# Optimization experiments

Hardware: AMD Instinct MI355X
Metric: run time of the kernel (lower is better)

The kernel has to match this reference:

```python
import math
import jax, jax.numpy as jnp
import numpy as np

GROUPS = 32
EPS = 1e-5


def setup_inputs() -> dict:
    key = jax.random.key(0)
    ks = jax.random.split(key, 4)
    B, C, H, W = 32, 512, 32, 32
    x = jax.random.normal(ks[0], (B, C, H, W), dtype=jnp.float32)
    norm_gamma = jnp.ones((C,), dtype=jnp.float32)
    norm_beta = jnp.zeros((C,), dtype=jnp.float32)
    qkv_w = jax.random.normal(ks[1], (3 * C, C), dtype=jnp.float32) / math.sqrt(C)
    qkv_b = jnp.zeros((3 * C,), dtype=jnp.float32)
    proj_w = jax.random.normal(ks[2], (C, C), dtype=jnp.float32) / math.sqrt(C)
    proj_b = jnp.zeros((C,), dtype=jnp.float32)
    return {"x": x, "norm_gamma": norm_gamma, "norm_beta": norm_beta,
            "qkv_w": qkv_w, "qkv_b": qkv_b, "proj_w": proj_w, "proj_b": proj_b}


def _group_norm(x, gamma, beta):
    B, C, H, W = x.shape
    xg = x.reshape(B, GROUPS, C // GROUPS, H, W)
    mean = xg.mean(axis=(2, 3, 4), keepdims=True)
    var = xg.var(axis=(2, 3, 4), keepdims=True)
    xn = ((xg - mean) * jax.lax.rsqrt(var + EPS)).reshape(B, C, H, W)
    return xn * gamma[None, :, None, None] + beta[None, :, None, None]


def reference(x, norm_gamma, norm_beta, qkv_w, qkv_b, proj_w, proj_b):
    B, C, H, W = x.shape
    h = _group_norm(x, norm_gamma, norm_beta)
    # 1x1 conv == channel matmul: [3C, C] x [B, C, H, W] -> [B, 3C, H, W]
    qkv = jnp.einsum('oc,bchw->bohw', qkv_w, h) + qkv_b[None, :, None, None]
    qkv = qkv.reshape(B, 3, C, H * W)
    q, k, v = qkv[:, 0], qkv[:, 1], qkv[:, 2]  # each [B, C, N]
    scale = 1.0 / math.sqrt(math.sqrt(C))
    w = jnp.einsum('bci,bcj->bij', q * scale, k * scale)  # [B, N, N]
    w = jax.nn.softmax(w, axis=-1)
    h = jnp.einsum('bij,bcj->bci', w, v).reshape(B, C, H, W)
    out = x + jnp.einsum('oc,bchw->bohw', proj_w, h) + proj_b[None, :, None, None]
    return out
```

## Files before the change

kernel.cpp:

```cpp
#include <hip/hip_runtime.h>

#define GROUPS 32
#define CPG    16
#define C_DIM  512
#define HW     1024
#define B_DIM  32

typedef __attribute__((ext_vector_type(8))) short bf16x8;
typedef __attribute__((ext_vector_type(4))) float f32x4;
typedef __attribute__((ext_vector_type(8))) unsigned short u16x8;

__device__ inline unsigned short f2bf(float f) {
  unsigned u = __builtin_bit_cast(unsigned, f);
  u += 0x7fff + ((u >> 16) & 1);
  return (unsigned short)(u >> 16);
}
__device__ inline float bf2f(unsigned short s) {
  return __builtin_bit_cast(float, ((unsigned)s) << 16);
}

__device__ inline void mfma16(f32x4& d, bf16x8 a, bf16x8 b) {
  asm("v_mfma_f32_16x16x32_bf16 %0, %1, %2, %0" : "+v"(d) : "v"(a), "v"(b));
}

__device__ inline void stage128x64(const unsigned short* g0, size_t rowStride,
                                   unsigned short* lds, int wave, int lane) {
  int r  = lane >> 3;
  int k8 = (lane & 7) * 8;
#pragma unroll
  for (int i = 0; i < 4; ++i) {
    const unsigned short* g = g0 + (size_t)(wave * 32 + i * 8 + r) * rowStride + k8;
    unsigned short* l = lds + (wave * 32 + i * 8) * 64;
    __builtin_amdgcn_global_load_lds((const __attribute__((address_space(1))) void*)g,
                                     (__attribute__((address_space(3))) void*)l, 16, 0, 0);
  }
}

__device__ inline void mfma_tile64(const unsigned short* As, const unsigned short* Bs,
                                   f32x4 acc[4][4], int lane, int wm, int wn) {
  int ar = (wm * 64 + (lane & 15)) * 64 + ((lane >> 4) << 3);
  int br = (wn * 64 + (lane & 15)) * 64 + ((lane >> 4) << 3);
#pragma unroll
  for (int kk = 0; kk < 64; kk += 32) {
    bf16x8 a[4], b[4];
#pragma unroll
    for (int mi = 0; mi < 4; ++mi) a[mi] = *(const bf16x8*)&As[ar + mi * 16 * 64 + kk];
#pragma unroll
    for (int ni = 0; ni < 4; ++ni) b[ni] = *(const bf16x8*)&Bs[br + ni * 16 * 64 + kk];
#pragma unroll
    for (int mi = 0; mi < 4; ++mi)
#pragma unroll
      for (int ni = 0; ni < 4; ++ni) mfma16(acc[mi][ni], a[mi], b[ni]);
  }
}

__global__ __launch_bounds__(256) void gn_stats_k(const float* __restrict__ x,
                                                  float* __restrict__ mean,
                                                  float* __restrict__ rstd) {
  int blk = blockIdx.x;
  const float4* p = (const float4*)(x + (size_t)blk * (CPG * HW));
  float s = 0.f, ss = 0.f;
  for (int i = threadIdx.x; i < CPG * HW / 4; i += 256) {
    float4 v = p[i];
    s  += v.x + v.y + v.z + v.w;
    ss += v.x * v.x + v.y * v.y + v.z * v.z + v.w * v.w;
  }
#pragma unroll
  for (int off = 32; off > 0; off >>= 1) {
    s  += __shfl_xor(s, off);
    ss += __shfl_xor(ss, off);
  }
  __shared__ float sm[8];
  int wave = threadIdx.x >> 6, lane = threadIdx.x & 63;
  if (lane == 0) { sm[wave] = s; sm[wave + 4] = ss; }
  __syncthreads();
  if (threadIdx.x == 0) {
    float S  = sm[0] + sm[1] + sm[2] + sm[3];
    float SS = sm[4] + sm[5] + sm[6] + sm[7];
    float mu  = S * (1.f / (CPG * HW));
    float var = SS * (1.f / (CPG * HW)) - mu * mu;
    mean[blk] = mu;
    rstd[blk] = rsqrtf(var + 1e-5f);
  }
}

__global__ __launch_bounds__(256) void prep_k(const float* __restrict__ qkv_w,
                                              const float* __restrict__ qkv_b,
                                              const float* __restrict__ proj_w,
                                              unsigned short* __restrict__ wq_bf,
                                              unsigned short* __restrict__ pw_bf,
                                              float* __restrict__ b_s) {
  const float SC = 0.21022410381342863f;
  int t = blockIdx.x * 256 + threadIdx.x;
  for (int i = t; i < 1536 * 512 / 4; i += gridDim.x * 256) {
    float4 w = *(const float4*)&qkv_w[i * 4];
    float sc = (i * 4 < 1024 * 512) ? SC : 1.f;
    ushort4 o;
    o.x = f2bf(w.x * sc); o.y = f2bf(w.y * sc); o.z = f2bf(w.z * sc); o.w = f2bf(w.w * sc);
    *(ushort4*)&wq_bf[i * 4] = o;
  }
  for (int i = t; i < 512 * 512 / 4; i += gridDim.x * 256) {
    float4 w = *(const float4*)&proj_w[i * 4];
    ushort4 o;
    o.x = f2bf(w.x); o.y = f2bf(w.y); o.z = f2bf(w.z); o.w = f2bf(w.w);
    *(ushort4*)&pw_bf[i * 4] = o;
  }
  if (t < 1536) b_s[t] = qkv_b[t] * (t < 1024 ? SC : 1.f);
}

__global__ __launch_bounds__(256) void gn_apply_t_k(const float* __restrict__ x,
                                                    const float* __restrict__ gamma,
                                                    const float* __restrict__ beta,
                                                    const float* __restrict__ mean,
                                                    const float* __restrict__ rstd,
                                                    unsigned short* __restrict__ hn_t) {
  __shared__ unsigned short Ls[64 * 68];
  int b = blockIdx.z, p0 = blockIdx.x * 64, c0 = blockIdx.y * 64;
  int tid = threadIdx.x;
  int c_loc = tid >> 4, p4 = (tid & 15) * 4;
#pragma unroll
  for (int cc = 0; cc < 4; ++cc) {
    int c = c_loc + cc * 16;
    int cg = c0 + c;
    float rs = rstd[b * GROUPS + (cg >> 4)];
    float ga = gamma[cg] * rs;
    float be = beta[cg] - mean[b * GROUPS + (cg >> 4)] * ga;
    float4 x4 = *(const float4*)&x[((size_t)b * C_DIM + cg) * HW + p0 + p4];
    ushort4 o;
    o.x = f2bf(x4.x * ga + be); o.y = f2bf(x4.y * ga + be);
    o.z = f2bf(x4.z * ga + be); o.w = f2bf(x4.w * ga + be);
    *(ushort4*)&Ls[c * 68 + p4] = o;
  }
  __syncthreads();
#pragma unroll
  for (int pass = 0; pass < 2; ++pass) {
    int cid = tid + pass * 256;
    int p = cid >> 3, c8 = cid & 7;
    u16x8 o;
#pragma unroll
    for (int u = 0; u < 8; ++u) o[u] = Ls[(c8 * 8 + u) * 68 + p];
    *(u16x8*)&hn_t[((size_t)b * HW + p0 + p) * C_DIM + c0 + c8 * 8] = o;
  }
}

__global__ __launch_bounds__(256) void qkv_gemm_k(
    const unsigned short* __restrict__ wq_bf, const unsigned short* __restrict__ hn_t,
    const float* __restrict__ b_s, unsigned short* __restrict__ q_t,
    unsigned short* __restrict__ k_t, unsigned short* __restrict__ vx) {
  __shared__ __align__(16) unsigned short As[128 * 64];
  __shared__ __align__(16) unsigned short Bs[128 * 64];
  int b = blockIdx.z, o0 = blockIdx.x * 128, p0 = blockIdx.y * 128;
  int tid = threadIdx.x, lane = tid & 63, wave = tid >> 6, wm = wave >> 1, wn = wave & 1;
  f32x4 acc[4][4] = {};
  const unsigned short* hb = hn_t + (size_t)b * HW * C_DIM;
  for (int kt = 0; kt < C_DIM; kt += 64) {
    __syncthreads();
    stage128x64(wq_bf + (size_t)o0 * C_DIM + kt, C_DIM, As, wave, lane);
    stage128x64(hb + (size_t)p0 * C_DIM + kt, C_DIM, Bs, wave, lane);
    __syncthreads();
    mfma_tile64(As, Bs, acc, lane, wm, wn);
  }
#pragma unroll
  for (int mi = 0; mi < 4; ++mi) {
    int obase = o0 + wm * 64 + mi * 16 + ((lane >> 4) << 2);
    float4 bias = *(const float4*)&b_s[obase];
#pragma unroll
    for (int ni = 0; ni < 4; ++ni) {
      int p = p0 + wn * 64 + ni * 16 + (lane & 15);
      if (o0 < 512) {
        ushort4 o;
        o.x = f2bf(acc[mi][ni][0] + bias.x); o.y = f2bf(acc[mi][ni][1] + bias.y);
        o.z = f2bf(acc[mi][ni][2] + bias.z); o.w = f2bf(acc[mi][ni][3] + bias.w);
        *(ushort4*)&q_t[((size_t)b * HW + p) * C_DIM + obase] = o;
      } else if (o0 < 1024) {
        ushort4 o;
        o.x = f2bf(acc[mi][ni][0] + bias.x); o.y = f2bf(acc[mi][ni][1] + bias.y);
        o.z = f2bf(acc[mi][ni][2] + bias.z); o.w = f2bf(acc[mi][ni][3] + bias.w);
        *(ushort4*)&k_t[((size_t)b * HW + p) * C_DIM + obase - 512] = o;
      } else {
        float bb[4] = {bias.x, bias.y, bias.z, bias.w};
#pragma unroll
        for (int r = 0; r < 4; ++r)
          vx[((size_t)b * C_DIM + obase - 1024 + r) * HW + p] = f2bf(acc[mi][ni][r] + bb[r]);
      }
    }
  }
}

__global__ __launch_bounds__(256) void qk_gemm_k(const unsigned short* __restrict__ q_t,
                                                 const unsigned short* __restrict__ k_t,
                                                 unsigned short* __restrict__ S) {
  __shared__ __align__(16) unsigned short As[128 * 64];
  __shared__ __align__(16) unsigned short Bs[128 * 64];
  int b = blockIdx.z, i0 = blockIdx.x * 128, j0 = blockIdx.y * 128;
  int tid = threadIdx.x, lane = tid & 63, wave = tid >> 6, wm = wave >> 1, wn = wave & 1;
  f32x4 acc[4][4] = {};
  const unsigned short* qb = q_t + (size_t)b * HW * C_DIM;
  const unsigned short* kb = k_t + (size_t)b * HW * C_DIM;
  for (int kt = 0; kt < C_DIM; kt += 64) {
    __syncthreads();
    stage128x64(qb + (size_t)i0 * C_DIM + kt, C_DIM, As, wave, lane);
    stage128x64(kb + (size_t)j0 * C_DIM + kt, C_DIM, Bs, wave, lane);
    __syncthreads();
    mfma_tile64(As, Bs, acc, lane, wm, wn);
  }
  unsigned short* Sb = S + (size_t)b * HW * HW;
#pragma unroll
  for (int mi = 0; mi < 4; ++mi)
#pragma unroll
    for (int ni = 0; ni < 4; ++ni) {
      int j = j0 + wn * 64 + ni * 16 + (lane & 15);
#pragma unroll
      for (int r = 0; r < 4; ++r) {
        int i = i0 + wm * 64 + mi * 16 + ((lane >> 4) << 2) + r;
        Sb[(size_t)i * HW + j] = f2bf(acc[mi][ni][r]);
      }
    }
}

__global__ __launch_bounds__(256) void softmax_k(unsigned short* __restrict__ S) {
  int row = blockIdx.x * 4 + (threadIdx.x >> 6);
  int lane = threadIdx.x & 63;
  unsigned short* rp = S + (size_t)row * HW + lane * 16;
  u16x8 a = *(const u16x8*)rp;
  u16x8 c = *(const u16x8*)(rp + 8);
  float f[16];
#pragma unroll
  for (int u = 0; u < 8; ++u) { f[u] = bf2f(a[u]); f[u + 8] = bf2f(c[u]); }
  float m = f[0];
#pragma unroll
  for (int u = 1; u < 16; ++u) m = fmaxf(m, f[u]);
#pragma unroll
  for (int off = 32; off > 0; off >>= 1) m = fmaxf(m, __shfl_xor(m, off));
  float s = 0.f;
#pragma unroll
  for (int u = 0; u < 16; ++u) { f[u] = __expf(f[u] - m); s += f[u]; }
#pragma unroll
  for (int off = 32; off > 0; off >>= 1) s += __shfl_xor(s, off);
  float inv = 1.0f / s;
#pragma unroll
  for (int u = 0; u < 8; ++u) { a[u] = f2bf(f[u] * inv); c[u] = f2bf(f[u + 8] * inv); }
  *(u16x8*)rp = a;
  *(u16x8*)(rp + 8) = c;
}

__global__ __launch_bounds__(256) void pv_gemm_k(const unsigned short* __restrict__ P,
                                                 const unsigned short* __restrict__ vx,
                                                 unsigned short* __restrict__ ha_t) {
  __shared__ __align__(16) unsigned short As[128 * 64];
  __shared__ __align__(16) unsigned short Bs[128 * 64];
  int b = blockIdx.z, i0 = blockIdx.x * 128, c0 = blockIdx.y * 128;
  int tid = threadIdx.x, lane = tid & 63, wave = tid >> 6, wm = wave >> 1, wn = wave & 1;
  f32x4 acc[4][4] = {};
  const unsigned short* Pb = P + (size_t)b * HW * HW;
  const unsigned short* vb = vx + (size_t)b * C_DIM * HW;
  for (int kt = 0; kt < HW; kt += 64) {
    __syncthreads();
    stage128x64(Pb + (size_t)i0 * HW + kt, HW, As, wave, lane);
    stage128x64(vb + (size_t)c0 * HW + kt, HW, Bs, wave, lane);
    __syncthreads();
    mfma_tile64(As, Bs, acc, lane, wm, wn);
  }
#pragma unroll
  for (int mi = 0; mi < 4; ++mi)
#pragma unroll
    for (int ni = 0; ni < 4; ++ni) {
      int c = c0 + wn * 64 + ni * 16 + (lane & 15);
#pragma unroll
      for (int r = 0; r < 4; ++r) {
        int i = i0 + wm * 64 + mi * 16 + ((lane >> 4) << 2) + r;
        ha_t[((size_t)b * HW + i) * C_DIM + c] = f2bf(acc[mi][ni][r]);
      }
    }
}

__global__ __launch_bounds__(256) void proj_gemm_k(const float* __restrict__ x,
                                                   const unsigned short* __restrict__ ha_t,
                                                   const unsigned short* __restrict__ pw_bf,
                                                   const float* __restrict__ proj_b,
                                                   float* __restrict__ out) {
  __shared__ __align__(16) unsigned short As[128 * 64];
  __shared__ __align__(16) unsigned short Bs[128 * 64];
  int b = blockIdx.z, o0 = blockIdx.x * 128, p0 = blockIdx.y * 128;
  int tid = threadIdx.x, lane = tid & 63, wave = tid >> 6, wm = wave >> 1, wn = wave & 1;
  f32x4 acc[4][4] = {};
  const unsigned short* hb = ha_t + (size_t)b * HW * C_DIM;
  for (int kt = 0; kt < C_DIM; kt += 64) {
    __syncthreads();
    stage128x64(pw_bf + (size_t)o0 * C_DIM + kt, C_DIM, As, wave, lane);
    stage128x64(hb + (size_t)p0 * C_DIM + kt, C_DIM, Bs, wave, lane);
    __syncthreads();
    mfma_tile64(As, Bs, acc, lane, wm, wn);
  }
  const float* xb = x + (size_t)b * C_DIM * HW;
  float* ob = out + (size_t)b * C_DIM * HW;
#pragma unroll
  for (int mi = 0; mi < 4; ++mi)
#pragma unroll
    for (int ni = 0; ni < 4; ++ni) {
      int p = p0 + wn * 64 + ni * 16 + (lane & 15);
#pragma unroll
      for (int r = 0; r < 4; ++r) {
        int o = o0 + wm * 64 + mi * 16 + ((lane >> 4) << 2) + r;
        size_t idx = (size_t)o * HW + p;
        ob[idx] = xb[idx] + acc[mi][ni][r] + proj_b[o];
      }
    }
}

extern "C" void kernel_launch(void* const* d_in, const int* in_sizes, int n_in,
                              void* d_out, int out_size, void* d_ws, size_t ws_size,
                              hipStream_t stream) {
  const float* x      = (const float*)d_in[0];
  const float* gamma  = (const float*)d_in[1];
  const float* beta   = (const float*)d_in[2];
  const float* qkv_w  = (const float*)d_in[3];
  const float* qkv_b  = (const float*)d_in[4];
  const float* proj_w = (const float*)d_in[5];
  const float* proj_b = (const float*)d_in[6];
  float* out = (float*)d_out;

  char* ws = (char*)d_ws;
  float* mean = (float*)ws;
  float* rstd = (float*)(ws + 4096);
  float* b_s  = (float*)(ws + 8192);
  unsigned short* pw_bf = (unsigned short*)(ws + 16384);
  unsigned short* wq_bf = (unsigned short*)(ws + 16384 + 512 * 512 * 2);
  unsigned short* vx   = (unsigned short*)(ws + ((size_t)4 << 20));
  unsigned short* ha_t = (unsigned short*)(ws + ((size_t)36 << 20));
  unsigned short* hn_t = (unsigned short*)(ws + ((size_t)68 << 20));
  unsigned short* S    = (unsigned short*)(ws + ((size_t)68 << 20));
  unsigned short* q_t  = (unsigned short*)d_out;
  unsigned short* k_t  = q_t + (size_t)B_DIM * HW * C_DIM;

  gn_stats_k<<<dim3(B_DIM * GROUPS), dim3(256), 0, stream>>>(x, mean, rstd);
  prep_k<<<dim3(512), dim3(256), 0, stream>>>(qkv_w, qkv_b, proj_w, wq_bf, pw_bf, b_s);
  gn_apply_t_k<<<dim3(16, 8, B_DIM), dim3(256), 0, stream>>>(x, gamma, beta, mean, rstd, hn_t);
  qkv_gemm_k<<<dim3(12, 8, B_DIM), dim3(256), 0, stream>>>(wq_bf, hn_t, b_s, q_t, k_t, vx);
  qk_gemm_k<<<dim3(8, 8, B_DIM), dim3(256), 0, stream>>>(q_t, k_t, S);
  softmax_k<<<dim3(B_DIM * HW / 4), dim3(256), 0, stream>>>(S);
  pv_gemm_k<<<dim3(8, 4, B_DIM), dim3(256), 0, stream>>>(S, vx, ha_t);
  proj_gemm_k<<<dim3(4, 8, B_DIM), dim3(256), 0, stream>>>(x, ha_t, pw_bf, proj_b, out);
}
```

Before: 395.9 us.

## Replace GEMMs with 256x256 double-buffered swizzled LDS pipeline on 512-thread blocks

All four GEMM kernels move from 128x128 tiles with single-buffered LDS to a shared 256x256 tile core run by 8 waves. The core double-buffers global-to-LDS loads with explicit vmcnt waits, applies an XOR swizzle to avoid LDS bank conflicts, and raises wave priority around the MFMA blocks. A block index remap groups tiles for L2 locality. The aim is to overlap memory with MFMA and raise arithmetic intensity, at the cost of 128KB dynamic LDS per block and more registers, which limits occupancy.

```diff
diff --git a/kernel.cpp b/kernel.cpp
--- a/kernel.cpp
+++ b/kernel.cpp
@@ -23,34 +23,109 @@
   asm("v_mfma_f32_16x16x32_bf16 %0, %1, %2, %0" : "+v"(d) : "v"(a), "v"(b));
 }
 
-__device__ inline void stage128x64(const unsigned short* g0, size_t rowStride,
-                                   unsigned short* lds, int wave, int lane) {
-  int r  = lane >> 3;
-  int k8 = (lane & 7) * 8;
-#pragma unroll
-  for (int i = 0; i < 4; ++i) {
-    const unsigned short* g = g0 + (size_t)(wave * 32 + i * 8 + r) * rowStride + k8;
-    unsigned short* l = lds + (wave * 32 + i * 8) * 64;
+__device__ __forceinline__ void stage_h(const unsigned short* g0, size_t stride,
+                                        unsigned short* ldsbase, int half, int w, int lane) {
+#pragma unroll
+  for (int i = 0; i < 2; ++i) {
+    int rbase = half * 128 + w * 16 + i * 8;
+    int row = rbase + (lane >> 3);
+    int chunk = (lane & 7) ^ (lane >> 3);
+    const unsigned short* g = g0 + (size_t)row * stride + chunk * 8;
+    unsigned short* l = ldsbase + rbase * 64;
     __builtin_amdgcn_global_load_lds((const __attribute__((address_space(1))) void*)g,
                                      (__attribute__((address_space(3))) void*)l, 16, 0, 0);
   }
 }
 
-__device__ inline void mfma_tile64(const unsigned short* As, const unsigned short* Bs,
-                                   f32x4 acc[4][4], int lane, int wm, int wn) {
-  int ar = (wm * 64 + (lane & 15)) * 64 + ((lane >> 4) << 3);
-  int br = (wn * 64 + (lane & 15)) * 64 + ((lane >> 4) << 3);
-#pragma unroll
-  for (int kk = 0; kk < 64; kk += 32) {
-    bf16x8 a[4], b[4];
-#pragma unroll
-    for (int mi = 0; mi < 4; ++mi) a[mi] = *(const bf16x8*)&As[ar + mi * 16 * 64 + kk];
-#pragma unroll
-    for (int ni = 0; ni < 4; ++ni) b[ni] = *(const bf16x8*)&Bs[br + ni * 16 * 64 + kk];
-#pragma unroll
-    for (int mi = 0; mi < 4; ++mi)
-#pragma unroll
-      for (int ni = 0; ni < 4; ++ni) mfma16(acc[mi][ni], a[mi], b[ni]);
+__device__ __forceinline__ void gemm256_core(const unsigned short* Ag, size_t sA,
+                                             const unsigned short* Bg, size_t sB,
+                                             int nkt, unsigned short* lds,
+                                             f32x4 (&acc)[2][4][4],
+                                             int lane, int w, int wm, int wn) {
+  unsigned short* Ab[2] = { lds, lds + 16384 };
+  unsigned short* Bb[2] = { lds + 32768, lds + 49152 };
+  stage_h(Bg, sB, Bb[0], 0, w, lane);
+  stage_h(Bg, sB, Bb[0], 1, w, lane);
+  stage_h(Ag, sA, Ab[0], 0, w, lane);
+  stage_h(Ag, sA, Ab[0], 1, w, lane);
+  int cur = 0;
+  for (int t = 0; t < nkt; ++t) {
+    const unsigned short* As = Ab[cur];
+    const unsigned short* Bs = Bb[cur];
+    const unsigned short* An = Ag + (size_t)(t + 1) * 64;
+    const unsigned short* Bn = Bg + (size_t)(t + 1) * 64;
+    bool last = (t == nkt - 1);
+    bf16x8 bfr[4][2];
+    if (!last) {
+      stage_h(Bn, sB, Bb[cur ^ 1], 0, w, lane);
+      stage_h(Bn, sB, Bb[cur ^ 1], 1, w, lane);
+      asm volatile("s_waitcnt vmcnt(6)" ::: "memory");
+    } else {
+      asm volatile("s_waitcnt vmcnt(2)" ::: "memory");
+    }
+    __builtin_amdgcn_s_barrier();
+    __builtin_amdgcn_sched_barrier(0);
+    {
+      int g4 = lane >> 4;
+      bf16x8 af[4][2];
+#pragma unroll
+      for (int ni = 0; ni < 4; ++ni) {
+        int r = wn * 64 + ni * 16 + (lane & 15);
+#pragma unroll
+        for (int kk = 0; kk < 2; ++kk)
+          bfr[ni][kk] = *(const bf16x8*)&Bs[r * 64 + (((kk * 4 + g4) ^ (r & 7)) << 3)];
+      }
+#pragma unroll
+      for (int mi = 0; mi < 4; ++mi) {
+        int r = wm * 64 + mi * 16 + (lane & 15);
+#pragma unroll
+        for (int kk = 0; kk < 2; ++kk)
+          af[mi][kk] = *(const bf16x8*)&As[r * 64 + (((kk * 4 + g4) ^ (r & 7)) << 3)];
+      }
+      __builtin_amdgcn_s_setprio(1);
+#pragma unroll
+      for (int kk = 0; kk < 2; ++kk)
+#pragma unroll
+        for (int mi = 0; mi < 4; ++mi)
+#pragma unroll
+          for (int ni = 0; ni < 4; ++ni)
+            mfma16(acc[0][mi][ni], af[mi][kk], bfr[ni][kk]);
+      __builtin_amdgcn_s_setprio(0);
+    }
+    if (!last) {
+      stage_h(An, sA, Ab[cur ^ 1], 0, w, lane);
+      stage_h(An, sA, Ab[cur ^ 1], 1, w, lane);
+      asm volatile("s_waitcnt vmcnt(8)" ::: "memory");
+    } else {
+      asm volatile("s_waitcnt vmcnt(0)" ::: "memory");
+    }
+    __builtin_amdgcn_s_barrier();
+    __builtin_amdgcn_sched_barrier(0);
+    {
+      int g4 = lane >> 4;
+      bf16x8 af[4][2];
+#pragma unroll
+      for (int mi = 0; mi < 4; ++mi) {
+        int r = 128 + wm * 64 + mi * 16 + (lane & 15);
+#pragma unroll
+        for (int kk = 0; kk < 2; ++kk)
+          af[mi][kk] = *(const bf16x8*)&As[r * 64 + (((kk * 4 + g4) ^ (r & 7)) << 3)];
+      }
+      __builtin_amdgcn_s_setprio(1);
+#pragma unroll
+      for (int kk = 0; kk < 2; ++kk)
+#pragma unroll
+        for (int mi = 0; mi < 4; ++mi)
+#pragma unroll
+          for (int ni = 0; ni < 4; ++ni)
+            mfma16(acc[1][mi][ni], af[mi][kk], bfr[ni][kk]);
+      __builtin_amdgcn_s_setprio(0);
+    }
+    asm volatile("s_waitcnt lgkmcnt(0)" ::: "memory");
+    __builtin_amdgcn_sched_barrier(0);
+    __builtin_amdgcn_s_barrier();
+    __builtin_amdgcn_sched_barrier(0);
+    cur ^= 1;
   }
 }
 
@@ -143,77 +218,74 @@
   }
 }
 
-__global__ __launch_bounds__(256) void qkv_gemm_k(
+__global__ __launch_bounds__(512, 2) void qkv_gemm_k(
     const unsigned short* __restrict__ wq_bf, const unsigned short* __restrict__ hn_t,
     const float* __restrict__ b_s, unsigned short* __restrict__ q_t,
     unsigned short* __restrict__ k_t, unsigned short* __restrict__ vx) {
-  __shared__ __align__(16) unsigned short As[128 * 64];
-  __shared__ __align__(16) unsigned short Bs[128 * 64];
-  int b = blockIdx.z, o0 = blockIdx.x * 128, p0 = blockIdx.y * 128;
-  int tid = threadIdx.x, lane = tid & 63, wave = tid >> 6, wm = wave >> 1, wn = wave & 1;
-  f32x4 acc[4][4] = {};
-  const unsigned short* hb = hn_t + (size_t)b * HW * C_DIM;
-  for (int kt = 0; kt < C_DIM; kt += 64) {
-    __syncthreads();
-    stage128x64(wq_bf + (size_t)o0 * C_DIM + kt, C_DIM, As, wave, lane);
-    stage128x64(hb + (size_t)p0 * C_DIM + kt, C_DIM, Bs, wave, lane);
-    __syncthreads();
-    mfma_tile64(As, Bs, acc, lane, wm, wn);
-  }
-#pragma unroll
-  for (int mi = 0; mi < 4; ++mi) {
-    int obase = o0 + wm * 64 + mi * 16 + ((lane >> 4) << 2);
-    float4 bias = *(const float4*)&b_s[obase];
-#pragma unroll
-    for (int ni = 0; ni < 4; ++ni) {
-      int p = p0 + wn * 64 + ni * 16 + (lane & 15);
-      if (o0 < 512) {
-        ushort4 o;
-        o.x = f2bf(acc[mi][ni][0] + bias.x); o.y = f2bf(acc[mi][ni][1] + bias.y);
-        o.z = f2bf(acc[mi][ni][2] + bias.z); o.w = f2bf(acc[mi][ni][3] + bias.w);
-        *(ushort4*)&q_t[((size_t)b * HW + p) * C_DIM + obase] = o;
-      } else if (o0 < 1024) {
-        ushort4 o;
-        o.x = f2bf(acc[mi][ni][0] + bias.x); o.y = f2bf(acc[mi][ni][1] + bias.y);
-        o.z = f2bf(acc[mi][ni][2] + bias.z); o.w = f2bf(acc[mi][ni][3] + bias.w);
-        *(ushort4*)&k_t[((size_t)b * HW + p) * C_DIM + obase - 512] = o;
-      } else {
-        float bb[4] = {bias.x, bias.y, bias.z, bias.w};
+  extern __shared__ unsigned short lds[];
+  constexpr int NX = 6, NXY = 24, CPX = NXY / 8;
+  int tgt = (blockIdx.x & 7) * CPX + (blockIdx.x >> 3);
+  int bx = tgt % NX, by = tgt / NX;
+  int b = blockIdx.z;
+  int tid = threadIdx.x, lane = tid & 63, w = tid >> 6, wm = w >> 2, wn = w & 3;
+  f32x4 acc[2][4][4] = {};
+  const unsigned short* Ag = wq_bf + (size_t)(bx * 256) * C_DIM;
+  const unsigned short* Bg = hn_t + ((size_t)b * HW + by * 256) * C_DIM;
+  gemm256_core(Ag, C_DIM, Bg, C_DIM, C_DIM / 64, lds, acc, lane, w, wm, wn);
+#pragma unroll
+  for (int s = 0; s < 2; ++s)
+#pragma unroll
+    for (int mi = 0; mi < 4; ++mi) {
+      int o = bx * 256 + s * 128 + wm * 64 + mi * 16 + ((lane >> 4) << 2);
+      float4 bv = *(const float4*)&b_s[o];
+      float bb[4] = {bv.x, bv.y, bv.z, bv.w};
+#pragma unroll
+      for (int ni = 0; ni < 4; ++ni) {
+        int p = by * 256 + wn * 64 + ni * 16 + (lane & 15);
+        if (bx < 2) {
+          ushort4 st;
+          st.x = f2bf(acc[s][mi][ni][0] + bb[0]); st.y = f2bf(acc[s][mi][ni][1] + bb[1]);
+          st.z = f2bf(acc[s][mi][ni][2] + bb[2]); st.w = f2bf(acc[s][mi][ni][3] + bb[3]);
+          *(ushort4*)&q_t[((size_t)b * HW + p) * C_DIM + o] = st;
+        } else if (bx < 4) {
+          ushort4 st;
+          st.x = f2bf(acc[s][mi][ni][0] + bb[0]); st.y = f2bf(acc[s][mi][ni][1] + bb[1]);
+          st.z = f2bf(acc[s][mi][ni][2] + bb[2]); st.w = f2bf(acc[s][mi][ni][3] + bb[3]);
+          *(ushort4*)&k_t[((size_t)b * HW + p) * C_DIM + (o - 512)] = st;
+        } else {
+#pragma unroll
+          for (int r = 0; r < 4; ++r)
+            vx[((size_t)b * C_DIM + (o - 1024) + r) * HW + p] = f2bf(acc[s][mi][ni][r] + bb[r]);
+        }
+      }
+    }
+}
+
+__global__ __launch_bounds__(512, 2) void qk_gemm_k(const unsigned short* __restrict__ q_t,
+                                                    const unsigned short* __restrict__ k_t,
+                                                    unsigned short* __restrict__ S) {
+  extern __shared__ unsigned short lds[];
+  constexpr int NX = 4, NXY = 16, CPX = NXY / 8;
+  int tgt = (blockIdx.x & 7) * CPX + (blockIdx.x >> 3);
+  int bx = tgt % NX, by = tgt / NX;
+  int b = blockIdx.z;
+  int tid = threadIdx.x, lane = tid & 63, w = tid >> 6, wm = w >> 2, wn = w & 3;
+  f32x4 acc[2][4][4] = {};
+  const unsigned short* Ag = q_t + ((size_t)b * HW + bx * 256) * C_DIM;
+  const unsigned short* Bg = k_t + ((size_t)b * HW + by * 256) * C_DIM;
+  gemm256_core(Ag, C_DIM, Bg, C_DIM, C_DIM / 64, lds, acc, lane, w, wm, wn);
+  unsigned short* Sb = S + (size_t)b * HW * HW;
+#pragma unroll
+  for (int s = 0; s < 2; ++s)
+#pragma unroll
+    for (int mi = 0; mi < 4; ++mi) {
+      int i0 = bx * 256 + s * 128 + wm * 64 + mi * 16 + ((lane >> 4) << 2);
+#pragma unroll
+      for (int ni = 0; ni < 4; ++ni) {
+        int j = by * 256 + wn * 64 + ni * 16 + (lane & 15);
 #pragma unroll
         for (int r = 0; r < 4; ++r)
-          vx[((size_t)b * C_DIM + obase - 1024 + r) * HW + p] = f2bf(acc[mi][ni][r] + bb[r]);
-      }
-    }
-  }
-}
-
-__global__ __launch_bounds__(256) void qk_gemm_k(const unsigned short* __restrict__ q_t,
-                                                 const unsigned short* __restrict__ k_t,
-                                                 unsigned short* __restrict__ S) {
-  __shared__ __align__(16) unsigned short As[128 * 64];
-  __shared__ __align__(16) unsigned short Bs[128 * 64];
-  int b = blockIdx.z, i0 = blockIdx.x * 128, j0 = blockIdx.y * 128;
-  int tid = threadIdx.x, lane = tid & 63, wave = tid >> 6, wm = wave >> 1, wn = wave & 1;
-  f32x4 acc[4][4] = {};
-  const unsigned short* qb = q_t + (size_t)b * HW * C_DIM;
-  const unsigned short* kb = k_t + (size_t)b * HW * C_DIM;
-  for (int kt = 0; kt < C_DIM; kt += 64) {
-    __syncthreads();
-    stage128x64(qb + (size_t)i0 * C_DIM + kt, C_DIM, As, wave, lane);
-    stage128x64(kb + (size_t)j0 * C_DIM + kt, C_DIM, Bs, wave, lane);
-    __syncthreads();
-    mfma_tile64(As, Bs, acc, lane, wm, wn);
-  }
-  unsigned short* Sb = S + (size_t)b * HW * HW;
-#pragma unroll
-  for (int mi = 0; mi < 4; ++mi)
-#pragma unroll
-    for (int ni = 0; ni < 4; ++ni) {
-      int j = j0 + wn * 64 + ni * 16 + (lane & 15);
-#pragma unroll
-      for (int r = 0; r < 4; ++r) {
-        int i = i0 + wm * 64 + mi * 16 + ((lane >> 4) << 2) + r;
-        Sb[(size_t)i * HW + j] = f2bf(acc[mi][ni][r]);
+          Sb[(size_t)(i0 + r) * HW + j] = f2bf(acc[s][mi][ni][r]);
       }
     }
 }
@@ -244,66 +316,66 @@
   *(u16x8*)(rp + 8) = c;
 }
 
-__global__ __launch_bounds__(256) void pv_gemm_k(const unsigned short* __restrict__ P,
-                                                 const unsigned short* __restrict__ vx,
-                                                 unsigned short* __restrict__ ha_t) {
-  __shared__ __align__(16) unsigned short As[128 * 64];
-  __shared__ __align__(16) unsigned short Bs[128 * 64];
-  int b = blockIdx.z, i0 = blockIdx.x * 128, c0 = blockIdx.y * 128;
-  int tid = threadIdx.x, lane = tid & 63, wave = tid >> 6, wm = wave >> 1, wn = wave & 1;
-  f32x4 acc[4][4] = {};
-  const unsigned short* Pb = P + (size_t)b * HW * HW;
-  const unsigned short* vb = vx + (size_t)b * C_DIM * HW;
-  for (int kt = 0; kt < HW; kt += 64) {
-    __syncthreads();
-    stage128x64(Pb + (size_t)i0 * HW + kt, HW, As, wave, lane);
-    stage128x64(vb + (size_t)c0 * HW + kt, HW, Bs, wave, lane);
-    __syncthreads();
-    mfma_tile64(As, Bs, acc, lane, wm, wn);
-  }
-#pragma unroll
-  for (int mi = 0; mi < 4; ++mi)
-#pragma unroll
-    for (int ni = 0; ni < 4; ++ni) {
-      int c = c0 + wn * 64 + ni * 16 + (lane & 15);
-#pragma unroll
-      for (int r = 0; r < 4; ++r) {
-        int i = i0 + wm * 64 + mi * 16 + ((lane >> 4) << 2) + r;
-        ha_t[((size_t)b * HW + i) * C_DIM + c] = f2bf(acc[mi][ni][r]);
-      }
-    }
-}
-
-__global__ __launch_bounds__(256) void proj_gemm_k(const float* __restrict__ x,
-                                                   const unsigned short* __restrict__ ha_t,
-                                                   const unsigned short* __restrict__ pw_bf,
-                                                   const float* __restrict__ proj_b,
-                                                   float* __restrict__ out) {
-  __shared__ __align__(16) unsigned short As[128 * 64];
-  __shared__ __align__(16) unsigned short Bs[128 * 64];
-  int b = blockIdx.z, o0 = blockIdx.x * 128, p0 = blockIdx.y * 128;
-  int tid = threadIdx.x, lane = tid & 63, wave = tid >> 6, wm = wave >> 1, wn = wave & 1;
-  f32x4 acc[4][4] = {};
-  const unsigned short* hb = ha_t + (size_t)b * HW * C_DIM;
-  for (int kt = 0; kt < C_DIM; kt += 64) {
-    __syncthreads();
-    stage128x64(pw_bf + (size_t)o0 * C_DIM + kt, C_DIM, As, wave, lane);
-    stage128x64(hb + (size_t)p0 * C_DIM + kt, C_DIM, Bs, wave, lane);
-    __syncthreads();
-    mfma_tile64(As, Bs, acc, lane, wm, wn);
-  }
+__global__ __launch_bounds__(512, 2) void pv_gemm_k(const unsigned short* __restrict__ P,
+                                                    const unsigned short* __restrict__ vx,
+                                                    unsigned short* __restrict__ ha_t) {
+  extern __shared__ unsigned short lds[];
+  constexpr int NX = 4, NXY = 8, CPX = NXY / 8;
+  int tgt = (blockIdx.x & 7) * CPX + (blockIdx.x >> 3);
+  int bx = tgt % NX, by = tgt / NX;
+  int b = blockIdx.z;
+  int tid = threadIdx.x, lane = tid & 63, w = tid >> 6, wm = w >> 2, wn = w & 3;
+  f32x4 acc[2][4][4] = {};
+  const unsigned short* Ag = P + (size_t)b * HW * HW + (size_t)(bx * 256) * HW;
+  const unsigned short* Bg = vx + (size_t)b * C_DIM * HW + (size_t)(by * 256) * HW;
+  gemm256_core(Ag, HW, Bg, HW, HW / 64, lds, acc, lane, w, wm, wn);
+#pragma unroll
+  for (int s = 0; s < 2; ++s)
+#pragma unroll
+    for (int mi = 0; mi < 4; ++mi) {
+      int i0 = bx * 256 + s * 128 + wm * 64 + mi * 16 + ((lane >> 4) << 2);
+#pragma unroll
+      for (int ni = 0; ni < 4; ++ni) {
+        int c = by * 256 + wn * 64 + ni * 16 + (lane & 15);
+#pragma unroll
+        for (int r = 0; r < 4; ++r)
+          ha_t[((size_t)b * HW + i0 + r) * C_DIM + c] = f2bf(acc[s][mi][ni][r]);
+      }
+    }
+}
+
+__global__ __launch_bounds__(512, 2) void proj_gemm_k(const float* __restrict__ x,
+                                                      const unsigned short* __restrict__ ha_t,
+                                                      const unsigned short* __restrict__ pw_bf,
+                                                      const float* __restrict__ proj_b,
+                                                      float* __restrict__ out) {
+  extern __shared__ unsigned short lds[];
+  constexpr int NX = 2, NXY = 8, CPX = NXY / 8;
+  int tgt = (blockIdx.x & 7) * CPX + (blockIdx.x >> 3);
+  int bx = tgt % NX, by = tgt / NX;
+  int b = blockIdx.z;
+  int tid = threadIdx.x, lane = tid & 63, w = tid >> 6, wm = w >> 2, wn = w & 3;
+  f32x4 acc[2][4][4] = {};
+  const unsigned short* Ag = pw_bf + (size_t)(bx * 256) * C_DIM;
+  const unsigned short* Bg = ha_t + ((size_t)b * HW + by * 256) * C_DIM;
+  gemm256_core(Ag, C_DIM, Bg, C_DIM, C_DIM / 64, lds, acc, lane, w, wm, wn);
   const float* xb = x + (size_t)b * C_DIM * HW;
   float* ob = out + (size_t)b * C_DIM * HW;
 #pragma unroll
-  for (int mi = 0; mi < 4; ++mi)
-#pragma unroll
-    for (int ni = 0; ni < 4; ++ni) {
-      int p = p0 + wn * 64 + ni * 16 + (lane & 15);
-#pragma unroll
-      for (int r = 0; r < 4; ++r) {
-        int o = o0 + wm * 64 + mi * 16 + ((lane >> 4) << 2) + r;
-        size_t idx = (size_t)o * HW + p;
-        ob[idx] = xb[idx] + acc[mi][ni][r] + proj_b[o];
+  for (int s = 0; s < 2; ++s)
+#pragma unroll
+    for (int mi = 0; mi < 4; ++mi) {
+      int o = bx * 256 + s * 128 + wm * 64 + mi * 16 + ((lane >> 4) << 2);
+      float4 pb4 = *(const float4*)&proj_b[o];
+      float pb[4] = {pb4.x, pb4.y, pb4.z, pb4.w};
+#pragma unroll
+      for (int ni = 0; ni < 4; ++ni) {
+        int p = by * 256 + wn * 64 + ni * 16 + (lane & 15);
+#pragma unroll
+        for (int r = 0; r < 4; ++r) {
+          size_t idx = (size_t)(o + r) * HW + p;
+          ob[idx] = xb[idx] + acc[s][mi][ni][r] + pb[r];
+        }
       }
     }
 }
@@ -333,12 +405,18 @@
   unsigned short* q_t  = (unsigned short*)d_out;
   unsigned short* k_t  = q_t + (size_t)B_DIM * HW * C_DIM;
 
+  const int SH = 131072;
+  hipFuncSetAttribute((const void*)qkv_gemm_k,  hipFuncAttributeMaxDynamicSharedMemorySize, SH);
+  hipFuncSetAttribute((const void*)qk_gemm_k,   hipFuncAttributeMaxDynamicSharedMemorySize, SH);
+  hipFuncSetAttribute((const void*)pv_gemm_k,   hipFuncAttributeMaxDynamicSharedMemorySize, SH);
+  hipFuncSetAttribute((const void*)proj_gemm_k, hipFuncAttributeMaxDynamicSharedMemorySize, SH);
+
   gn_stats_k<<<dim3(B_DIM * GROUPS), dim3(256), 0, stream>>>(x, mean, rstd);
   prep_k<<<dim3(512), dim3(256), 0, stream>>>(qkv_w, qkv_b, proj_w, wq_bf, pw_bf, b_s);
   gn_apply_t_k<<<dim3(16, 8, B_DIM), dim3(256), 0, stream>>>(x, gamma, beta, mean, rstd, hn_t);
-  qkv_gemm_k<<<dim3(12, 8, B_DIM), dim3(256), 0, stream>>>(wq_bf, hn_t, b_s, q_t, k_t, vx);
-  qk_gemm_k<<<dim3(8, 8, B_DIM), dim3(256), 0, stream>>>(q_t, k_t, S);
+  qkv_gemm_k<<<dim3(24, 1, B_DIM), dim3(512), SH, stream>>>(wq_bf, hn_t, b_s, q_t, k_t, vx);
+  qk_gemm_k<<<dim3(16, 1, B_DIM), dim3(512), SH, stream>>>(q_t, k_t, S);
   softmax_k<<<dim3(B_DIM * HW / 4), dim3(256), 0, stream>>>(S);
-  pv_gemm_k<<<dim3(8, 4, B_DIM), dim3(256), 0, stream>>>(S, vx, ha_t);
-  proj_gemm_k<<<dim3(4, 8, B_DIM), dim3(256), 0, stream>>>(x, ha_t, pw_bf, proj_b, out);
-}
+  pv_gemm_k<<<dim3(8, 1, B_DIM), dim3(512), SH, stream>>>(S, vx, ha_t);
+  proj_gemm_k<<<dim3(8, 1, B_DIM), dim3(512), SH, stream>>>(x, ha_t, pw_bf, proj_b, out);
+}
```

New measurement: 403.6 us. About the same (+1.9%).

## Fuse QK, softmax and PV into a flash-attention kernel; remap block order

Applied to the files above, without the earlier changes.

Replaces the separate QK^T GEMM, softmax and PV GEMM kernels with one flash-style kernel. Each 512-thread block keeps Q fragments in registers, streams K and V tiles into swizzled LDS with global_load_lds, and applies an online softmax with running max and sum. This avoids writing and re-reading the 64 MB bf16 score matrix and drops two launches. The QKV and projection GEMMs are also launched on a 1D grid with an XCD-aware block remap to improve L2 locality. The cost is heavy register pressure (32 accumulators plus 16 Q fragments), about 145 KB of dynamic LDS per block, only 256 blocks in flight, and load/compute serialised by the barrier placement.

```diff
diff --git a/kernel.cpp b/kernel.cpp
--- a/kernel.cpp
+++ b/kernel.cpp
@@ -149,7 +149,10 @@
     unsigned short* __restrict__ k_t, unsigned short* __restrict__ vx) {
   __shared__ __align__(16) unsigned short As[128 * 64];
   __shared__ __align__(16) unsigned short Bs[128 * 64];
-  int b = blockIdx.z, o0 = blockIdx.x * 128, p0 = blockIdx.y * 128;
+  int lin = blockIdx.x;
+  int tgt = (lin & 7) * 384 + (lin >> 3);
+  int b = tgt / 96, rem = tgt % 96, by = rem / 12, bx = rem % 12;
+  int o0 = bx * 128, p0 = by * 128;
   int tid = threadIdx.x, lane = tid & 63, wave = tid >> 6, wm = wave >> 1, wn = wave & 1;
   f32x4 acc[4][4] = {};
   const unsigned short* hb = hn_t + (size_t)b * HW * C_DIM;
@@ -187,91 +190,150 @@
   }
 }
 
-__global__ __launch_bounds__(256) void qk_gemm_k(const unsigned short* __restrict__ q_t,
-                                                 const unsigned short* __restrict__ k_t,
-                                                 unsigned short* __restrict__ S) {
-  __shared__ __align__(16) unsigned short As[128 * 64];
-  __shared__ __align__(16) unsigned short Bs[128 * 64];
-  int b = blockIdx.z, i0 = blockIdx.x * 128, j0 = blockIdx.y * 128;
-  int tid = threadIdx.x, lane = tid & 63, wave = tid >> 6, wm = wave >> 1, wn = wave & 1;
-  f32x4 acc[4][4] = {};
-  const unsigned short* qb = q_t + (size_t)b * HW * C_DIM;
+#define FK_K 0
+#define FK_V 32768
+#define FK_P 65536
+#define FK_SC 73728
+#define FK_LI 73984
+__global__ __launch_bounds__(512, 2) void flash_k(const unsigned short* __restrict__ q_t,
+                                                  const unsigned short* __restrict__ k_t,
+                                                  const unsigned short* __restrict__ vx,
+                                                  unsigned short* __restrict__ ha_t) {
+  extern __shared__ unsigned short lds[];
+  unsigned short* k_lds = lds + FK_K;
+  unsigned short* v_lds = lds + FK_V;
+  unsigned short* p_lds = lds + FK_P;
+  float* sc_lds = (float*)(lds + FK_SC);
+  float* li_lds = (float*)(lds + FK_LI);
+
+  int lin = blockIdx.x;
+  int tgt = (lin & 7) * 32 + (lin >> 3);
+  int b = tgt >> 3, itile = tgt & 7;
+  int i0 = itile * 128;
+  int tid = threadIdx.x, lane = tid & 63, w = tid >> 6;
+  int L4 = lane & 15, hi = lane >> 4;
+
+  bf16x8 qf[16];
+  {
+    const unsigned short* qrow = q_t + ((size_t)b * HW + i0 + w * 16 + L4) * C_DIM + hi * 8;
+#pragma unroll
+    for (int cc = 0; cc < 16; ++cc) qf[cc] = *(const bf16x8*)&qrow[cc * 32];
+  }
+
+  f32x4 acc[8][4] = {};
+  float m_run[4] = {-3.0e38f, -3.0e38f, -3.0e38f, -3.0e38f};
+  float l_run[4] = {0.f, 0.f, 0.f, 0.f};
+
   const unsigned short* kb = k_t + (size_t)b * HW * C_DIM;
-  for (int kt = 0; kt < C_DIM; kt += 64) {
-    __syncthreads();
-    stage128x64(qb + (size_t)i0 * C_DIM + kt, C_DIM, As, wave, lane);
-    stage128x64(kb + (size_t)j0 * C_DIM + kt, C_DIM, Bs, wave, lane);
-    __syncthreads();
-    mfma_tile64(As, Bs, acc, lane, wm, wn);
-  }
-  unsigned short* Sb = S + (size_t)b * HW * HW;
-#pragma unroll
-  for (int mi = 0; mi < 4; ++mi)
+  const unsigned short* vb0 = vx + (size_t)b * C_DIM * HW;
+
+  auto stageK = [&](int t) {
+#pragma unroll
+    for (int rr = 0; rr < 8; ++rr) {
+      int j = rr * 8 + w;
+      const unsigned short* g = kb + (size_t)(t * 64 + j) * C_DIM + ((lane ^ (j & 7)) * 8);
+      unsigned short* l = k_lds + j * 512;
+      __builtin_amdgcn_global_load_lds((const __attribute__((address_space(1))) void*)g,
+                                       (__attribute__((address_space(3))) void*)l, 16, 0, 0);
+    }
+  };
+  auto stageV = [&](int t) {
+#pragma unroll
+    for (int rr = 0; rr < 8; ++rr) {
+      int c = rr * 64 + w * 8 + (lane >> 3);
+      const unsigned short* g = vb0 + (size_t)c * HW + t * 64 + (((lane & 7) ^ (lane >> 3)) * 8);
+      unsigned short* l = v_lds + (rr * 64 + w * 8) * 64;
+      __builtin_amdgcn_global_load_lds((const __attribute__((address_space(1))) void*)g,
+                                       (__attribute__((address_space(3))) void*)l, 16, 0, 0);
+    }
+  };
+
+  stageK(0);
+  stageV(0);
+  __syncthreads();
+
+  for (int t = 0; t < 16; ++t) {
+    f32x4 s[4] = {};
+#pragma unroll
+    for (int cc = 0; cc < 16; ++cc) {
+      bf16x8 kf[4];
+#pragma unroll
+      for (int ni = 0; ni < 4; ++ni) {
+        int j = ni * 16 + L4;
+        int jc = (cc * 4 + hi) ^ (j & 7);
+        kf[ni] = *(const bf16x8*)&k_lds[j * 512 + jc * 8];
+      }
+#pragma unroll
+      for (int ni = 0; ni < 4; ++ni) mfma16(s[ni], qf[cc], kf[ni]);
+    }
+    float sc_f[4];
+#pragma unroll
+    for (int r = 0; r < 4; ++r) {
+      float rmax = fmaxf(fmaxf(s[0][r], s[1][r]), fmaxf(s[2][r], s[3][r]));
+#pragma unroll
+      for (int mk = 1; mk < 16; mk <<= 1) rmax = fmaxf(rmax, __shfl_xor(rmax, mk));
+      float mnew = fmaxf(m_run[r], rmax);
+      sc_f[r] = __expf(m_run[r] - mnew);
+      float rsum = 0.f;
+      int i_loc = w * 16 + hi * 4 + r;
+      int sw = (i_loc & 7) << 3;
+#pragma unroll
+      for (int ni = 0; ni < 4; ++ni) {
+        float pv = __expf(s[ni][r] - mnew);
+        rsum += pv;
+        p_lds[i_loc * 64 + ((ni * 16 + L4) ^ sw)] = f2bf(pv);
+      }
+#pragma unroll
+      for (int mk = 1; mk < 16; mk <<= 1) rsum += __shfl_xor(rsum, mk);
+      l_run[r] = l_run[r] * sc_f[r] + rsum;
+      m_run[r] = mnew;
+      if (L4 == 0) sc_lds[i_loc] = sc_f[r];
+    }
+    __syncthreads();
+    if (t < 15) stageK(t + 1);
+#pragma unroll
+    for (int mi = 0; mi < 8; ++mi) {
+      f32x4 scv = *(const f32x4*)&sc_lds[mi * 16 + hi * 4];
+#pragma unroll
+      for (int ni = 0; ni < 4; ++ni) acc[mi][ni] *= scv;
+    }
+#pragma unroll
+    for (int kk = 0; kk < 2; ++kk) {
+      bf16x8 vf[4];
+#pragma unroll
+      for (int ni = 0; ni < 4; ++ni) {
+        int c = w * 64 + ni * 16 + L4;
+        int jc = (hi + kk * 4) ^ (c & 7);
+        vf[ni] = *(const bf16x8*)&v_lds[(c & 511) * 64 + jc * 8];
+      }
+#pragma unroll
+      for (int mi = 0; mi < 8; ++mi) {
+        int ir = mi * 16 + L4;
+        int jc = (hi + kk * 4) ^ (ir & 7);
+        bf16x8 pa = *(const bf16x8*)&p_lds[ir * 64 + jc * 8];
+#pragma unroll
+        for (int ni = 0; ni < 4; ++ni) mfma16(acc[mi][ni], pa, vf[ni]);
+      }
+    }
+    __syncthreads();
+    if (t < 15) stageV(t + 1);
+  }
+#pragma unroll
+  for (int r = 0; r < 4; ++r)
+    if (L4 == 0) li_lds[w * 16 + hi * 4 + r] = 1.0f / l_run[r];
+  __syncthreads();
+#pragma unroll
+  for (int mi = 0; mi < 8; ++mi) {
+    f32x4 li = *(const f32x4*)&li_lds[mi * 16 + hi * 4];
+    size_t gi = (size_t)b * HW + i0 + mi * 16 + hi * 4;
 #pragma unroll
     for (int ni = 0; ni < 4; ++ni) {
-      int j = j0 + wn * 64 + ni * 16 + (lane & 15);
-#pragma unroll
-      for (int r = 0; r < 4; ++r) {
-        int i = i0 + wm * 64 + mi * 16 + ((lane >> 4) << 2) + r;
-        Sb[(size_t)i * HW + j] = f2bf(acc[mi][ni][r]);
-      }
-    }
-}
-
-__global__ __launch_bounds__(256) void softmax_k(unsigned short* __restrict__ S) {
-  int row = blockIdx.x * 4 + (threadIdx.x >> 6);
-  int lane = threadIdx.x & 63;
-  unsigned short* rp = S + (size_t)row * HW + lane * 16;
-  u16x8 a = *(const u16x8*)rp;
-  u16x8 c = *(const u16x8*)(rp + 8);
-  float f[16];
-#pragma unroll
-  for (int u = 0; u < 8; ++u) { f[u] = bf2f(a[u]); f[u + 8] = bf2f(c[u]); }
-  float m = f[0];
-#pragma unroll
-  for (int u = 1; u < 16; ++u) m = fmaxf(m, f[u]);
-#pragma unroll
-  for (int off = 32; off > 0; off >>= 1) m = fmaxf(m, __shfl_xor(m, off));
-  float s = 0.f;
-#pragma unroll
-  for (int u = 0; u < 16; ++u) { f[u] = __expf(f[u] - m); s += f[u]; }
-#pragma unroll
-  for (int off = 32; off > 0; off >>= 1) s += __shfl_xor(s, off);
-  float inv = 1.0f / s;
-#pragma unroll
-  for (int u = 0; u < 8; ++u) { a[u] = f2bf(f[u] * inv); c[u] = f2bf(f[u + 8] * inv); }
-  *(u16x8*)rp = a;
-  *(u16x8*)(rp + 8) = c;
-}
-
-__global__ __launch_bounds__(256) void pv_gemm_k(const unsigned short* __restrict__ P,
-                                                 const unsigned short* __restrict__ vx,
-                                                 unsigned short* __restrict__ ha_t) {
-  __shared__ __align__(16) unsigned short As[128 * 64];
-  __shared__ __align__(16) unsigned short Bs[128 * 64];
-  int b = blockIdx.z, i0 = blockIdx.x * 128, c0 = blockIdx.y * 128;
-  int tid = threadIdx.x, lane = tid & 63, wave = tid >> 6, wm = wave >> 1, wn = wave & 1;
-  f32x4 acc[4][4] = {};
-  const unsigned short* Pb = P + (size_t)b * HW * HW;
-  const unsigned short* vb = vx + (size_t)b * C_DIM * HW;
-  for (int kt = 0; kt < HW; kt += 64) {
-    __syncthreads();
-    stage128x64(Pb + (size_t)i0 * HW + kt, HW, As, wave, lane);
-    stage128x64(vb + (size_t)c0 * HW + kt, HW, Bs, wave, lane);
-    __syncthreads();
-    mfma_tile64(As, Bs, acc, lane, wm, wn);
-  }
-#pragma unroll
-  for (int mi = 0; mi < 4; ++mi)
-#pragma unroll
-    for (int ni = 0; ni < 4; ++ni) {
-      int c = c0 + wn * 64 + ni * 16 + (lane & 15);
-#pragma unroll
-      for (int r = 0; r < 4; ++r) {
-        int i = i0 + wm * 64 + mi * 16 + ((lane >> 4) << 2) + r;
-        ha_t[((size_t)b * HW + i) * C_DIM + c] = f2bf(acc[mi][ni][r]);
-      }
-    }
+      int c = w * 64 + ni * 16 + L4;
+#pragma unroll
+      for (int r = 0; r < 4; ++r)
+        ha_t[(gi + r) * C_DIM + c] = f2bf(acc[mi][ni][r] * li[r]);
+    }
+  }
 }
 
 __global__ __launch_bounds__(256) void proj_gemm_k(const float* __restrict__ x,
@@ -281,7 +343,10 @@
                                                    float* __restrict__ out) {
   __shared__ __align__(16) unsigned short As[128 * 64];
   __shared__ __align__(16) unsigned short Bs[128 * 64];
-  int b = blockIdx.z, o0 = blockIdx.x * 128, p0 = blockIdx.y * 128;
+  int lin = blockIdx.x;
+  int tgt = (lin & 7) * 128 + (lin >> 3);
+  int b = tgt / 32, rem = tgt % 32, by = rem / 4, bx = rem % 4;
+  int o0 = bx * 128, p0 = by * 128;
   int tid = threadIdx.x, lane = tid & 63, wave = tid >> 6, wm = wave >> 1, wn = wave & 1;
   f32x4 acc[4][4] = {};
   const unsigned short* hb = ha_t + (size_t)b * HW * C_DIM;
@@ -329,16 +394,16 @@
   unsigned short* vx   = (unsigned short*)(ws + ((size_t)4 << 20));
   unsigned short* ha_t = (unsigned short*)(ws + ((size_t)36 << 20));
   unsigned short* hn_t = (unsigned short*)(ws + ((size_t)68 << 20));
-  unsigned short* S    = (unsigned short*)(ws + ((size_t)68 << 20));
   unsigned short* q_t  = (unsigned short*)d_out;
   unsigned short* k_t  = q_t + (size_t)B_DIM * HW * C_DIM;
+
+  const int FSH = 148480;
+  hipFuncSetAttribute((const void*)flash_k, hipFuncAttributeMaxDynamicSharedMemorySize, FSH);
 
   gn_stats_k<<<dim3(B_DIM * GROUPS), dim3(256), 0, stream>>>(x, mean, rstd);
   prep_k<<<dim3(512), dim3(256), 0, stream>>>(qkv_w, qkv_b, proj_w, wq_bf, pw_bf, b_s);
   gn_apply_t_k<<<dim3(16, 8, B_DIM), dim3(256), 0, stream>>>(x, gamma, beta, mean, rstd, hn_t);
-  qkv_gemm_k<<<dim3(12, 8, B_DIM), dim3(256), 0, stream>>>(wq_bf, hn_t, b_s, q_t, k_t, vx);
-  qk_gemm_k<<<dim3(8, 8, B_DIM), dim3(256), 0, stream>>>(q_t, k_t, S);
-  softmax_k<<<dim3(B_DIM * HW / 4), dim3(256), 0, stream>>>(S);
-  pv_gemm_k<<<dim3(8, 4, B_DIM), dim3(256), 0, stream>>>(S, vx, ha_t);
-  proj_gemm_k<<<dim3(4, 8, B_DIM), dim3(256), 0, stream>>>(x, ha_t, pw_bf, proj_b, out);
-}
+  qkv_gemm_k<<<dim3(3072), dim3(256), 0, stream>>>(wq_bf, hn_t, b_s, q_t, k_t, vx);
+  flash_k<<<dim3(256), dim3(512), FSH, stream>>>(q_t, k_t, vx, ha_t);
+  proj_gemm_k<<<dim3(1024), dim3(256), 0, stream>>>(x, ha_t, pw_bf, proj_b, out);
+}
```

Result: slower. 520.2 us (+31.4%).
